# Optimization experiments

Measured on AMD Instinct MI355X. Metric: run time of the kernel, lower is better.

## Reference

```python
import jax, jax.numpy as jnp
import numpy as np

DIM = 1024
NUM_HEADS = 16
HEAD_DIM = DIM // NUM_HEADS


def setup_inputs() -> dict:
    key = jax.random.key(0)
    ks = jax.random.split(key, 5)
    B, T = 2, 2048
    x = jax.random.normal(ks[0], (B, T, DIM), dtype=jnp.float32)
    s = 1.0 / np.sqrt(DIM)
    W_qkv = jax.random.normal(ks[1], (DIM, 3 * DIM), dtype=jnp.float32) * s
    b_qkv = jnp.zeros((3 * DIM,), dtype=jnp.float32)
    W_out = jax.random.normal(ks[2], (DIM, DIM), dtype=jnp.float32) * s
    b_out = jnp.zeros((DIM,), dtype=jnp.float32)
    return {"x": x, "W_qkv": W_qkv, "b_qkv": b_qkv, "W_out": W_out, "b_out": b_out}


def reference(x, W_qkv, b_qkv, W_out, b_out):
    B, T, D = x.shape
    H, Hd = NUM_HEADS, HEAD_DIM
    qkv = x @ W_qkv + b_qkv                       # [B,T,3D]
    qkv = qkv.reshape(B, T, 3, H, Hd)
    q = jnp.transpose(qkv[:, :, 0], (0, 2, 1, 3))  # [B,H,T,Hd]
    k = jnp.transpose(qkv[:, :, 1], (0, 2, 1, 3))
    v = jnp.transpose(qkv[:, :, 2], (0, 2, 1, 3))
    att = jnp.einsum('bhqd,bhkd->bhqk', q, k) / np.sqrt(Hd)  # [B,H,T,T]
    causal = jnp.tril(jnp.ones((T, T), dtype=bool))
    att = jnp.where(causal[None, None], att, -jnp.inf)
    att = jax.nn.softmax(att, axis=-1)
    out = jnp.einsum('bhqk,bhkd->bhqd', att, v)   # [B,H,T,Hd]
    out = jnp.transpose(out, (0, 2, 1, 3)).reshape(B, T, D)
    return out @ W_out + b_out
```

## Files before the change

kernel.cpp:

```cpp
#include <hip/hip_runtime.h>
#include <hip/hip_bf16.h>

typedef unsigned short u16;
typedef __attribute__((ext_vector_type(8))) short short8;
typedef __attribute__((ext_vector_type(4))) float f32x4;
typedef __attribute__((ext_vector_type(4))) unsigned short u16x4;

#define LOG2E 1.44269504088896340736f
#define QSCALE_F 0.18033688011112042f


__device__ __forceinline__ void gl_lds16(const void* g, void* l) {
  __builtin_amdgcn_global_load_lds(
      (__attribute__((address_space(1))) void*)g,
      (__attribute__((address_space(3))) void*)l, 16, 0, 0);
}

__device__ __forceinline__ float exp2_fast(float x) {
#if __has_builtin(__builtin_amdgcn_exp2f)
  return __builtin_amdgcn_exp2f(x);
#else
  return exp2f(x);
#endif
}

__device__ __forceinline__ u16 f2bf(float f) {
  union { float f; unsigned int i; } v;
  v.f = f;
  unsigned int r = v.i + 0x7fffu + ((v.i >> 16) & 1u);
  return (u16)(r >> 16);
}

__device__ __forceinline__ unsigned int pack_bf2(float lo, float hi) {
  union { __hip_bfloat162 h2; unsigned int u; } c;
  c.h2 = __float22bfloat162_rn(make_float2(lo, hi));
  return c.u;
}


__global__ __launch_bounds__(256) void prep_kernel(
    const float4* __restrict__ x, u16x4* __restrict__ xb,
    const float* __restrict__ Wqkv, u16* __restrict__ WqkvT,
    const float* __restrict__ Wout, u16* __restrict__ WoutT) {
  __shared__ u16 t[64][65];
  int bid = blockIdx.x, tid = threadIdx.x;
  if (bid < 4096) {
    int i = bid * 256 + tid;
    float4 v = x[i];
    u16x4 o;
    o.x = f2bf(v.x); o.y = f2bf(v.y); o.z = f2bf(v.z); o.w = f2bf(v.w);
    xb[i] = o;
    return;
  }
  const float* W;
  u16* WT;
  int K = 1024, N, bxx, byy;
  if (bid < 4864) {
    int tt = bid - 4096;
    W = Wqkv; WT = WqkvT; N = 3072; bxx = tt % 48; byy = tt / 48;
  } else {
    int tt = bid - 4864;
    W = Wout; WT = WoutT; N = 1024; bxx = tt % 16; byy = tt / 16;
  }
  int r0 = byy * 64, c0 = bxx * 64;
  int tx = tid & 63, ty = tid >> 6;
  for (int r = ty; r < 64; r += 4)
    t[r][tx] = f2bf(W[(size_t)(r0 + r) * N + c0 + tx]);
  __syncthreads();
  for (int r = ty; r < 64; r += 4)
    WT[(size_t)(c0 + r) * K + r0 + tx] = t[tx][r];
}


template <bool OUT_F32, int BM, int BN, bool QSC>
__global__ __launch_bounds__(512, 1) void gemm8_kernel(
    const u16* __restrict__ A, const u16* __restrict__ Bt,
    const float* __restrict__ bias, void* __restrict__ Cout,
    int M, int N, int K) {
  constexpr int MI = BM / 32;
  constexpr int NJ = BN / 64;
  constexpr int CH_A = BM / 8;
  constexpr int CH_B = BN / 8;
  constexpr int PER_W = (CH_A + CH_B) / 8;
  __shared__ u16 LDS[2][(BM + BN) * 64];
  int tid = threadIdx.x;
  int w = tid >> 6, lane = tid & 63, l15 = lane & 15, quad = lane >> 4;
  int bid = blockIdx.y * gridDim.x + blockIdx.x;
  int swz = ((bid & 7) << 5) | (bid >> 3);
  int bx = swz % gridDim.x, by = swz / gridDim.x;
  int m0 = by * BM, n0 = bx * BN;
  int wm = (w & 1) * (BM / 2), wn = (w >> 1) * (BN / 4);

  f32x4 acc[MI][NJ];
#pragma unroll
  for (int i = 0; i < MI; ++i)
#pragma unroll
    for (int j = 0; j < NJ; ++j) {
      f32x4 z = {0.f, 0.f, 0.f, 0.f};
      acc[i][j] = z;
    }

  int r8 = lane >> 3;
  int sw = ((lane & 7) ^ r8) * 8;

  const u16* srcp[PER_W];
  int dsto[PER_W];
#pragma unroll
  for (int i = 0; i < PER_W; ++i) {
    int c = w * PER_W + i;
    if (c < CH_A) {
      srcp[i] = A + (size_t)(m0 + c * 8 + r8) * K + sw;
    } else {
      srcp[i] = Bt + (size_t)(n0 + (c - CH_A) * 8 + r8) * K + sw;
    }
    dsto[i] = c * 512;
  }

  int nt = K >> 6;
#pragma unroll
  for (int i = 0; i < PER_W; ++i) gl_lds16(srcp[i], &LDS[0][dsto[i]]);

  for (int t = 0; t < nt; ++t) {
    asm volatile("s_waitcnt vmcnt(0)" ::: "memory");
    __builtin_amdgcn_s_barrier();
    asm volatile("" ::: "memory");
    int cur = t & 1;
    if (t + 1 < nt) {
      int koff = (t + 1) << 6;
#pragma unroll
      for (int i = 0; i < PER_W; ++i)
        gl_lds16(srcp[i] + koff, &LDS[cur ^ 1][dsto[i]]);
    }
    const u16* As = &LDS[cur][0];
    const u16* Bs = &LDS[cur][CH_A * 512];
#pragma unroll
    for (int kh = 0; kh < 2; ++kh) {
      short8 af[MI], bf[NJ];
#pragma unroll
      for (int i = 0; i < MI; ++i) {
        int R = wm + i * 16 + l15;
        af[i] = *(const short8*)(As + R * 64 +
                                 ((kh * 32 + quad * 8) ^ ((R & 7) * 8)));
      }
#pragma unroll
      for (int j = 0; j < NJ; ++j) {
        int R = wn + j * 16 + l15;
        bf[j] = *(const short8*)(Bs + R * 64 +
                                 ((kh * 32 + quad * 8) ^ ((R & 7) * 8)));
      }
#pragma unroll
      for (int i = 0; i < MI; ++i)
#pragma unroll
        for (int j = 0; j < NJ; ++j)
          acc[i][j] = __builtin_amdgcn_mfma_f32_16x16x32_bf16(af[i], bf[j],
                                                              acc[i][j], 0, 0, 0);
    }
  }

  float bv[NJ];
#pragma unroll
  for (int j = 0; j < NJ; ++j) bv[j] = bias[n0 + wn + j * 16 + l15];
#pragma unroll
  for (int i = 0; i < MI; ++i)
#pragma unroll
    for (int j = 0; j < NJ; ++j) {
      int col = n0 + wn + j * 16 + l15;
      bool doq = QSC && (col < 1024);
#pragma unroll
      for (int r = 0; r < 4; ++r) {
        int row = m0 + wm + i * 16 + quad * 4 + r;
        float val = acc[i][j][r] + bv[j];
        if (doq) val *= QSCALE_F;
        if (OUT_F32)
          ((float*)Cout)[(size_t)row * N + col] = val;
        else
          ((u16*)Cout)[(size_t)row * N + col] = f2bf(val);
      }
    }
}


__global__ __launch_bounds__(256, 2) void flash_kernel(
    const u16* __restrict__ qkv, u16* __restrict__ att) {
  __shared__ unsigned int SH[10240];

  int tid = threadIdx.x;
  int wq = tid >> 6;
  int lane = tid & 63, l15 = lane & 15, quad = lane >> 4;
  int bid = blockIdx.x;
  int ch = bid >> 8;
  int c = bid & 255;
  int p = c >> 5, bh = c & 31, b = bh >> 4, h = bh & 15;
  const int st0 = 15 - p, st1 = p;
  const int n0t = 2 * st0 + ch + 1;
  const int n1t = 2 * st1 + ch + 1;
  const int ntot = n0t + n1t;

  const u16* base = qkv + (size_t)b * 2048 * 3072 + h * 64;
  const u16* kb = base + 1024;
  const u16* vb = base + 2048;

  const int krow = tid >> 3, h7 = tid & 7;
  const int swk = (h7 ^ (krow & 7)) * 8;

  short8 qf[2][2];
#pragma unroll
  for (int t = 0; t < 2; ++t) {
    int stt = t ? st1 : st0;
    const u16* qtb =
        base + (size_t)(stt * 128 + ch * 64 + wq * 16 + l15) * 3072;
    qf[t][0] = *(const short8*)(qtb + quad * 8);
    qf[t][1] = *(const short8*)(qtb + 32 + quad * 8);
  }

  gl_lds16(kb + (size_t)krow * 3072 + swk, (char*)SH + wq * 1024);
  gl_lds16(kb + (size_t)(32 + krow) * 3072 + swk,
           (char*)SH + 4096 + wq * 1024);
  uint4 vr0 = *(const uint4*)(vb + (size_t)(2 * krow) * 3072 + h7 * 8);
  uint4 vr1 = *(const uint4*)(vb + (size_t)(2 * krow + 1) * 3072 + h7 * 8);

  f32x4 o[2][4];
#pragma unroll
  for (int t = 0; t < 2; ++t)
#pragma unroll
    for (int jd = 0; jd < 4; ++jd) {
      f32x4 z = {0.f, 0.f, 0.f, 0.f};
      o[t][jd] = z;
    }
  float lsum[2] = {0.f, 0.f};

  const int psw = (l15 & 7) << 2;
  unsigned int* Pw = SH + 8192 + wq * 512;
  const int qq = (wq << 4) + l15;

  for (int i = 0; i < ntot; ++i) {
    int t = (i >= n0t) ? 1 : 0;
    int kt = t ? i - n0t : i;
    int kml = t ? (n1t - 1) : (n0t - 1);
    unsigned int* KsH = SH + (i & 1) * 2048;
    unsigned int* VtH = SH + 4096 + (i & 1) * 2048;

    {
      const u16* av = (const u16*)&vr0;
      const u16* bvp = (const u16*)&vr1;
#pragma unroll
      for (int jj = 0; jj < 8; ++jj) {
        int d = h7 * 8 + jj;
        VtH[32 * d + (krow ^ ((jj ^ h7) << 2))] =
            (unsigned int)av[jj] | ((unsigned int)bvp[jj] << 16);
      }
    }
    asm volatile("s_waitcnt lgkmcnt(0)" ::: "memory");
    __builtin_amdgcn_s_barrier();
    asm volatile("" ::: "memory");

    if (i + 1 < ntot) {
      int t2 = (i + 1 >= n0t) ? 1 : 0;
      int kt2 = t2 ? (i + 1 - n0t) : (i + 1);
      int kn = kt2 * 64;
      unsigned int* Ksn = SH + ((i + 1) & 1) * 2048;
      gl_lds16(kb + (size_t)(kn + krow) * 3072 + swk, (char*)Ksn + wq * 1024);
      gl_lds16(kb + (size_t)(kn + 32 + krow) * 3072 + swk,
               (char*)Ksn + 4096 + wq * 1024);
      vr0 = *(const uint4*)(vb + (size_t)(kn + 2 * krow) * 3072 + h7 * 8);
      vr1 = *(const uint4*)(vb + (size_t)(kn + 2 * krow + 1) * 3072 + h7 * 8);
    }

    bool domask = (kt == kml);
    f32x4 s[4];
#pragma unroll
    for (int jn = 0; jn < 4; ++jn) {
      f32x4 z = {-16.f, -16.f, -16.f, -16.f};
      s[jn] = z;
    }
    __builtin_amdgcn_s_setprio(1);
#pragma unroll
    for (int ss = 0; ss < 2; ++ss) {
      short8 a = qf[t][ss];
#pragma unroll
      for (int jn = 0; jn < 4; ++jn) {
        int row = jn * 16 + l15;
        short8 bk = *(const short8*)&KsH[32 * row + ((16 * ss + 4 * quad) ^
                                                     ((row & 7) << 2))];
        s[jn] = __builtin_amdgcn_mfma_f32_16x16x32_bf16(bk, a, s[jn], 0, 0, 0);
      }
    }
    __builtin_amdgcn_s_setprio(0);

    {
      float pvv[4][4];
      if (domask) {
#pragma unroll
        for (int jn = 0; jn < 4; ++jn)
#pragma unroll
          for (int r = 0; r < 4; ++r) {
            float e = exp2_fast(s[jn][r]);
            if (jn * 16 + quad * 4 + r > qq) e = 0.f;
            pvv[jn][r] = e;
          }
      } else {
#pragma unroll
        for (int jn = 0; jn < 4; ++jn)
#pragma unroll
          for (int r = 0; r < 4; ++r)
            pvv[jn][r] = exp2_fast(s[jn][r]);
      }
      float t0 = (pvv[0][0] + pvv[0][1]) + (pvv[0][2] + pvv[0][3]);
      float t1 = (pvv[1][0] + pvv[1][1]) + (pvv[1][2] + pvv[1][3]);
      float t2 = (pvv[2][0] + pvv[2][1]) + (pvv[2][2] + pvv[2][3]);
      float t3 = (pvv[3][0] + pvv[3][1]) + (pvv[3][2] + pvv[3][3]);
      lsum[t] += (t0 + t1) + (t2 + t3);
#pragma unroll
      for (int jn = 0; jn < 4; ++jn) {
        uint2 dd = make_uint2(pack_bf2(pvv[jn][0], pvv[jn][1]),
                              pack_bf2(pvv[jn][2], pvv[jn][3]));
        *(uint2*)&Pw[32 * l15 + (((jn << 3) + (quad << 1)) ^ psw)] = dd;
      }
    }

    __builtin_amdgcn_s_setprio(1);
#pragma unroll
    for (int ss = 0; ss < 2; ++ss) {
      short8 pf = *(const short8*)&Pw[32 * l15 +
                                      (((ss << 4) + (quad << 2)) ^ psw)];
#pragma unroll
      for (int jd = 0; jd < 4; ++jd) {
        int vrow = jd * 16 + l15;
        int f = (vrow & 7) ^ ((vrow >> 3) & 7);
        short8 bvv = *(const short8*)&VtH[32 * vrow +
                                          (((ss << 4) + (quad << 2)) ^ (f << 2))];
        o[t][jd] =
            __builtin_amdgcn_mfma_f32_16x16x32_bf16(bvv, pf, o[t][jd], 0, 0, 0);
      }
    }
    __builtin_amdgcn_s_setprio(0);
  }

#pragma unroll
  for (int t = 0; t < 2; ++t) {
    float v = lsum[t];
    v += __shfl_xor(v, 16, 64);
    v += __shfl_xor(v, 32, 64);
    float inv = 1.f / v;
    int stt = t ? st1 : st0;
    size_t row = (size_t)b * 2048 + stt * 128 + ch * 64 + wq * 16 + l15;
    u16* orow = att + row * 1024 + h * 64 + quad * 4;
#pragma unroll
    for (int jd = 0; jd < 4; ++jd) {
      uint2 dd = make_uint2(pack_bf2(o[t][jd][0] * inv, o[t][jd][1] * inv),
                            pack_bf2(o[t][jd][2] * inv, o[t][jd][3] * inv));
      *(uint2*)(orow + jd * 16) = dd;
    }
  }
}


extern "C" void kernel_launch(void* const* d_in, const int* in_sizes, int n_in,
                              void* d_out, int out_size, void* d_ws,
                              size_t ws_size, hipStream_t stream) {
  const float* x = (const float*)d_in[0];
  const float* Wqkv = (const float*)d_in[1];
  const float* bqkv = (const float*)d_in[2];
  const float* Wout = (const float*)d_in[3];
  const float* bout = (const float*)d_in[4];
  float* out = (float*)d_out;

  char* ws = (char*)d_ws;
  u16* WqkvT = (u16*)(ws);
  u16* WoutT = (u16*)(ws + 6291456);
  u16* qkv = (u16*)(ws + 8388608);
  u16* attn = (u16*)(ws + 33554432);
  u16* xb = (u16*)(ws + 41943040);

  prep_kernel<<<5120, 256, 0, stream>>>((const float4*)x, (u16x4*)xb, Wqkv,
                                        WqkvT, Wout, WoutT);
  gemm8_kernel<false, 256, 192, true><<<dim3(16, 16), 512, 0, stream>>>(
      xb, WqkvT, bqkv, (void*)qkv, 4096, 3072, 1024);
  flash_kernel<<<512, 256, 0, stream>>>(qkv, attn);
  gemm8_kernel<true, 128, 128, false><<<dim3(8, 32), 512, 0, stream>>>(
      attn, WoutT, bout, (void*)out, 4096, 1024, 1024);
}
```

Baseline: 172.2 us.

## Restructure flash kernel to 512-thread blocks over 128-row query tiles

Each flash block now has 8 waves covering one 128-row query tile, instead of 4 waves handling two paired 64-row tiles. Work is balanced by block ordering rather than by pairing short and long tiles. K/V tiles are loaded 64 rows at a time with a triple-buffered K ring, and the softmax row sum is computed by an MFMA against a ones vector rather than scalar adds plus shuffles. This raises waves per block and removes the pairing loop overhead, but waves 0-3 idle on the last diagonal tile and LDS use per block grows.

```diff
diff --git a/kernel.cpp b/kernel.cpp
--- a/kernel.cpp
+++ b/kernel.cpp
@@ -180,21 +180,24 @@
 }
 
 
-__global__ __launch_bounds__(256, 2) void flash_kernel(
+__global__ __launch_bounds__(512, 4) void flash_kernel(
     const u16* __restrict__ qkv, u16* __restrict__ att) {
-  __shared__ unsigned int SH[10240];
+  __shared__ unsigned int SH[14336];
 
   int tid = threadIdx.x;
   int wq = tid >> 6;
   int lane = tid & 63, l15 = lane & 15, quad = lane >> 4;
   int bid = blockIdx.x;
-  int ch = bid >> 8;
-  int c = bid & 255;
-  int p = c >> 5, bh = c & 31, b = bh >> 4, h = bh & 15;
-  const int st0 = 15 - p, st1 = p;
-  const int n0t = 2 * st0 + ch + 1;
-  const int n1t = 2 * st1 + ch + 1;
-  const int ntot = n0t + n1t;
+  int s, bh;
+  if (bid < 256) {
+    s = bid >> 5;
+    bh = bid & 31;
+  } else {
+    s = 15 - ((bid - 256) >> 5);
+    bh = (bid - 256) & 31;
+  }
+  int b = bh >> 4, h = bh & 15;
+  const int nt = 2 * s + 2;
 
   const u16* base = qkv + (size_t)b * 2048 * 3072 + h * 64;
   const u16* kb = base + 1024;
@@ -203,86 +206,81 @@
   const int krow = tid >> 3, h7 = tid & 7;
   const int swk = (h7 ^ (krow & 7)) * 8;
 
-  short8 qf[2][2];
-#pragma unroll
-  for (int t = 0; t < 2; ++t) {
-    int stt = t ? st1 : st0;
-    const u16* qtb =
-        base + (size_t)(stt * 128 + ch * 64 + wq * 16 + l15) * 3072;
-    qf[t][0] = *(const short8*)(qtb + quad * 8);
-    qf[t][1] = *(const short8*)(qtb + 32 + quad * 8);
+  short8 qf[2];
+  {
+    const u16* qtb = base + (size_t)(s * 128 + wq * 16 + l15) * 3072;
+    qf[0] = *(const short8*)(qtb + quad * 8);
+    qf[1] = *(const short8*)(qtb + 32 + quad * 8);
   }
 
   gl_lds16(kb + (size_t)krow * 3072 + swk, (char*)SH + wq * 1024);
-  gl_lds16(kb + (size_t)(32 + krow) * 3072 + swk,
-           (char*)SH + 4096 + wq * 1024);
-  uint4 vr0 = *(const uint4*)(vb + (size_t)(2 * krow) * 3072 + h7 * 8);
-  uint4 vr1 = *(const uint4*)(vb + (size_t)(2 * krow + 1) * 3072 + h7 * 8);
-
-  f32x4 o[2][4];
-#pragma unroll
-  for (int t = 0; t < 2; ++t)
-#pragma unroll
-    for (int jd = 0; jd < 4; ++jd) {
-      f32x4 z = {0.f, 0.f, 0.f, 0.f};
-      o[t][jd] = z;
-    }
-  float lsum[2] = {0.f, 0.f};
+  uint4 vr = *(const uint4*)(vb + (size_t)krow * 3072 + h7 * 8);
+
+  f32x4 o[4];
+#pragma unroll
+  for (int jd = 0; jd < 4; ++jd) {
+    f32x4 z = {0.f, 0.f, 0.f, 0.f};
+    o[jd] = z;
+  }
+  f32x4 l4 = {0.f, 0.f, 0.f, 0.f};
+  const short8 ones = {(short)0x3F80, (short)0x3F80, (short)0x3F80,
+                       (short)0x3F80, (short)0x3F80, (short)0x3F80,
+                       (short)0x3F80, (short)0x3F80};
 
   const int psw = (l15 & 7) << 2;
-  unsigned int* Pw = SH + 8192 + wq * 512;
-  const int qq = (wq << 4) + l15;
-
-  for (int i = 0; i < ntot; ++i) {
-    int t = (i >= n0t) ? 1 : 0;
-    int kt = t ? i - n0t : i;
-    int kml = t ? (n1t - 1) : (n0t - 1);
-    unsigned int* KsH = SH + (i & 1) * 2048;
-    unsigned int* VtH = SH + 4096 + (i & 1) * 2048;
+  unsigned int* Pw = SH + 10240 + wq * 512;
+  const int kp2 = krow >> 1, kb1 = krow & 1;
+
+  int b3 = 0;
+  for (int kt = 0; kt < nt; ++kt) {
+    unsigned int* KsH = SH + b3 * 2048;
+    unsigned int* VtH = SH + 6144 + (kt & 1) * 2048;
 
     {
-      const u16* av = (const u16*)&vr0;
-      const u16* bvp = (const u16*)&vr1;
+      const u16* av = (const u16*)&vr;
+      u16* vt16 = (u16*)VtH;
 #pragma unroll
       for (int jj = 0; jj < 8; ++jj) {
         int d = h7 * 8 + jj;
-        VtH[32 * d + (krow ^ ((jj ^ h7) << 2))] =
-            (unsigned int)av[jj] | ((unsigned int)bvp[jj] << 16);
-      }
-    }
+        vt16[64 * d + 2 * (kp2 ^ ((jj ^ h7) << 2)) + kb1] = av[jj];
+      }
+    }
+
+    int nb3 = b3 + 1;
+    if (nb3 == 3) nb3 = 0;
+    if (kt + 1 < nt) {
+      gl_lds16(kb + (size_t)((kt + 1) * 64 + krow) * 3072 + swk,
+               (char*)(SH + nb3 * 2048) + wq * 1024);
+      vr = *(const uint4*)(vb + (size_t)((kt + 1) * 64 + krow) * 3072 + h7 * 8);
+    }
+    b3 = nb3;
+
     asm volatile("s_waitcnt lgkmcnt(0)" ::: "memory");
     __builtin_amdgcn_s_barrier();
     asm volatile("" ::: "memory");
 
-    if (i + 1 < ntot) {
-      int t2 = (i + 1 >= n0t) ? 1 : 0;
-      int kt2 = t2 ? (i + 1 - n0t) : (i + 1);
-      int kn = kt2 * 64;
-      unsigned int* Ksn = SH + ((i + 1) & 1) * 2048;
-      gl_lds16(kb + (size_t)(kn + krow) * 3072 + swk, (char*)Ksn + wq * 1024);
-      gl_lds16(kb + (size_t)(kn + 32 + krow) * 3072 + swk,
-               (char*)Ksn + 4096 + wq * 1024);
-      vr0 = *(const uint4*)(vb + (size_t)(kn + 2 * krow) * 3072 + h7 * 8);
-      vr1 = *(const uint4*)(vb + (size_t)(kn + 2 * krow + 1) * 3072 + h7 * 8);
-    }
-
-    bool domask = (kt == kml);
-    f32x4 s[4];
+    bool lastt = (kt == nt - 1);
+    if (lastt && wq < 4) continue;
+    bool domask = lastt || ((kt == nt - 2) && wq < 4);
+    int qq = lastt ? ((wq - 4) * 16 + l15) : (wq * 16 + l15);
+
+    f32x4 sacc[4];
 #pragma unroll
     for (int jn = 0; jn < 4; ++jn) {
       f32x4 z = {-16.f, -16.f, -16.f, -16.f};
-      s[jn] = z;
+      sacc[jn] = z;
     }
     __builtin_amdgcn_s_setprio(1);
 #pragma unroll
     for (int ss = 0; ss < 2; ++ss) {
-      short8 a = qf[t][ss];
+      short8 a = qf[ss];
 #pragma unroll
       for (int jn = 0; jn < 4; ++jn) {
         int row = jn * 16 + l15;
         short8 bk = *(const short8*)&KsH[32 * row + ((16 * ss + 4 * quad) ^
                                                      ((row & 7) << 2))];
-        s[jn] = __builtin_amdgcn_mfma_f32_16x16x32_bf16(bk, a, s[jn], 0, 0, 0);
+        sacc[jn] = __builtin_amdgcn_mfma_f32_16x16x32_bf16(bk, a, sacc[jn],
+                                                           0, 0, 0);
       }
     }
     __builtin_amdgcn_s_setprio(0);
@@ -294,7 +292,7 @@
         for (int jn = 0; jn < 4; ++jn)
 #pragma unroll
           for (int r = 0; r < 4; ++r) {
-            float e = exp2_fast(s[jn][r]);
+            float e = exp2_fast(sacc[jn][r]);
             if (jn * 16 + quad * 4 + r > qq) e = 0.f;
             pvv[jn][r] = e;
           }
@@ -303,13 +301,8 @@
         for (int jn = 0; jn < 4; ++jn)
 #pragma unroll
           for (int r = 0; r < 4; ++r)
-            pvv[jn][r] = exp2_fast(s[jn][r]);
-      }
-      float t0 = (pvv[0][0] + pvv[0][1]) + (pvv[0][2] + pvv[0][3]);
-      float t1 = (pvv[1][0] + pvv[1][1]) + (pvv[1][2] + pvv[1][3]);
-      float t2 = (pvv[2][0] + pvv[2][1]) + (pvv[2][2] + pvv[2][3]);
-      float t3 = (pvv[3][0] + pvv[3][1]) + (pvv[3][2] + pvv[3][3]);
-      lsum[t] += (t0 + t1) + (t2 + t3);
+            pvv[jn][r] = exp2_fast(sacc[jn][r]);
+      }
 #pragma unroll
       for (int jn = 0; jn < 4; ++jn) {
         uint2 dd = make_uint2(pack_bf2(pvv[jn][0], pvv[jn][1]),
@@ -323,34 +316,27 @@
     for (int ss = 0; ss < 2; ++ss) {
       short8 pf = *(const short8*)&Pw[32 * l15 +
                                       (((ss << 4) + (quad << 2)) ^ psw)];
+      l4 = __builtin_amdgcn_mfma_f32_16x16x32_bf16(ones, pf, l4, 0, 0, 0);
 #pragma unroll
       for (int jd = 0; jd < 4; ++jd) {
         int vrow = jd * 16 + l15;
         int f = (vrow & 7) ^ ((vrow >> 3) & 7);
         short8 bvv = *(const short8*)&VtH[32 * vrow +
                                           (((ss << 4) + (quad << 2)) ^ (f << 2))];
-        o[t][jd] =
-            __builtin_amdgcn_mfma_f32_16x16x32_bf16(bvv, pf, o[t][jd], 0, 0, 0);
+        o[jd] = __builtin_amdgcn_mfma_f32_16x16x32_bf16(bvv, pf, o[jd], 0, 0, 0);
       }
     }
     __builtin_amdgcn_s_setprio(0);
   }
 
-#pragma unroll
-  for (int t = 0; t < 2; ++t) {
-    float v = lsum[t];
-    v += __shfl_xor(v, 16, 64);
-    v += __shfl_xor(v, 32, 64);
-    float inv = 1.f / v;
-    int stt = t ? st1 : st0;
-    size_t row = (size_t)b * 2048 + stt * 128 + ch * 64 + wq * 16 + l15;
-    u16* orow = att + row * 1024 + h * 64 + quad * 4;
-#pragma unroll
-    for (int jd = 0; jd < 4; ++jd) {
-      uint2 dd = make_uint2(pack_bf2(o[t][jd][0] * inv, o[t][jd][1] * inv),
-                            pack_bf2(o[t][jd][2] * inv, o[t][jd][3] * inv));
-      *(uint2*)(orow + jd * 16) = dd;
-    }
+  float inv = 1.f / l4[0];
+  size_t row = (size_t)b * 2048 + s * 128 + wq * 16 + l15;
+  u16* orow = att + row * 1024 + h * 64 + quad * 4;
+#pragma unroll
+  for (int jd = 0; jd < 4; ++jd) {
+    uint2 dd = make_uint2(pack_bf2(o[jd][0] * inv, o[jd][1] * inv),
+                          pack_bf2(o[jd][2] * inv, o[jd][3] * inv));
+    *(uint2*)(orow + jd * 16) = dd;
   }
 }
 
@@ -376,7 +362,7 @@
                                         WqkvT, Wout, WoutT);
   gemm8_kernel<false, 256, 192, true><<<dim3(16, 16), 512, 0, stream>>>(
       xb, WqkvT, bqkv, (void*)qkv, 4096, 3072, 1024);
-  flash_kernel<<<512, 256, 0, stream>>>(qkv, attn);
+  flash_kernel<<<512, 512, 0, stream>>>(qkv, attn);
   gemm8_kernel<true, 128, 128, false><<<dim3(8, 32), 512, 0, stream>>>(
       attn, WoutT, bout, (void*)out, 4096, 1024, 1024);
 }
```

Measured after the change: 168.9 us. No clear change (-1.9%).
